# Kernel optimization log

Measured on AMD Instinct MI355X. Metric: run time of the kernel, lower is better.

## Reference

```python
import jax, jax.numpy as jnp
import numpy as np

EPS_IN = 1e-5   # torch InstanceNorm2d default eps
EPS_VAR = 1e-6  # clamp floor on attention-weighted variance


def _inorm(x):
    # x: (b, c, t); InstanceNorm2d with affine=False normalizes over spatial dims
    m = x.mean(axis=-1, keepdims=True)
    v = x.var(axis=-1, keepdims=True)  # biased variance, matches torch eval-mode IN
    return (x - m) / jnp.sqrt(v + EPS_IN)


def setup_inputs() -> dict:
    key = jax.random.key(0)
    ks = jax.random.split(key, 9)
    b, t, d = 4, 4096, 256
    sc = 1.0 / np.sqrt(d).astype(np.float32)
    return {
        "fc": jax.random.normal(ks[0], (b, t, d), jnp.float32),
        "fs": jax.random.normal(ks[1], (b, t, d), jnp.float32),
        "fcs": jax.random.normal(ks[2], (b, t, d), jnp.float32),
        "Wf": jax.random.normal(ks[3], (d, d), jnp.float32) * sc,
        "bf": jax.random.normal(ks[4], (d,), jnp.float32) * 0.01,
        "Wg": jax.random.normal(ks[5], (d, d), jnp.float32) * sc,
        "bg": jax.random.normal(ks[6], (d,), jnp.float32) * 0.01,
        "Wh": jax.random.normal(ks[7], (d, d), jnp.float32) * sc,
        "bh": jax.random.normal(ks[8], (d,), jnp.float32) * 0.01,
    }


def reference(fc, fs, fcs, Wf, bf, Wg, bg, Wh, bh):
    # (b, t, d) -> channel-first flat (b, d, t); 1x1 conv == per-token linear
    fc_t = jnp.swapaxes(fc, 1, 2)
    fs_t = jnp.swapaxes(fs, 1, 2)
    fcs_t = jnp.swapaxes(fcs, 1, 2)

    Q = jnp.einsum('oc,bct->bto', Wf, _inorm(fc_t)) + bf                 # (b,t,d)
    K = jnp.einsum('oc,bct->bot', Wg, _inorm(fs_t)) + bg[None, :, None]  # (b,d,t)
    V = jnp.einsum('oc,bct->bto', Wh, fs_t) + bh                         # (b,t,d)

    A = jax.nn.softmax(jnp.einsum('btd,bdu->btu', Q, K), axis=-1)        # (b,t,t)
    M = jnp.einsum('btu,bud->btd', A, V)                                 # mean
    Var = jnp.einsum('btu,bud->btd', A, V * V) - M * M                   # E[v^2]-E[v]^2
    S = jnp.sqrt(jnp.maximum(Var, EPS_VAR))

    out_t = jnp.swapaxes(S, 1, 2) * _inorm(fcs_t) + jnp.swapaxes(M, 1, 2)  # (b,d,t)
    return jnp.swapaxes(out_t, 1, 2)  # (b, t, d)
```

## Files before the change

kernel.cpp:

```cpp
#include <hip/hip_runtime.h>
#include <math.h>

#define B 4
#define T 4096
#define D 256
#define NCH 16
#define CHT (T / NCH)
#define KC 32
#define NCHUNK (T / KC)

typedef __attribute__((ext_vector_type(8))) _Float16 half8;
typedef __attribute__((ext_vector_type(4))) _Float16 half4;
typedef __attribute__((ext_vector_type(4))) float f32x4;

__global__ __launch_bounds__(256) void k_stats_part(
    const float* __restrict__ fc, const float* __restrict__ fs,
    const float* __restrict__ fcs, float* __restrict__ part)
{
    int blk = blockIdx.x;
    int tensor = blk / (B * NCH);
    int rem = blk % (B * NCH);
    int b = rem / NCH, ch = rem % NCH;
    const float* x = (tensor == 0) ? fc : ((tensor == 1) ? fs : fcs);
    int c = threadIdx.x;
    const float* p = x + ((size_t)b * T + (size_t)ch * CHT) * D + c;
    float s = 0.f, ss = 0.f;
    for (int t = 0; t < CHT; ++t) {
        float v = p[(size_t)t * D];
        s += v; ss += v * v;
    }
    float* o = part + (((size_t)tensor * B + b) * NCH + ch) * 2 * D;
    o[c] = s;
    o[D + c] = ss;
}

__global__ __launch_bounds__(256) void k_stats_final(
    const float* __restrict__ part, float* __restrict__ stats)
{
    int blk = blockIdx.x;
    int tensor = blk / B, b = blk % B;
    int c = threadIdx.x;
    const float* pp = part + (((size_t)tensor * B + b) * NCH) * 2 * D;
    float s = 0.f, ss = 0.f;
    for (int ch = 0; ch < NCH; ++ch) {
        s  += pp[(size_t)ch * 2 * D + c];
        ss += pp[(size_t)ch * 2 * D + D + c];
    }
    float mean = s / (float)T;
    float var  = ss / (float)T - mean * mean;
    float rstd = rsqrtf(var + 1e-5f);
    float* st = stats + (size_t)tensor * 2 * B * D;
    st[(size_t)b * D + c]          = mean;
    st[(size_t)B * D + b * D + c]  = rstd;
}

__global__ __launch_bounds__(256) void k_wprep(
    const float* __restrict__ Wf, const float* __restrict__ Wg,
    const float* __restrict__ Wh, _Float16* __restrict__ Whi,
    _Float16* __restrict__ Wlo)
{
    int blk = blockIdx.x;
    int which = blk >> 8, row = blk & 255;
    const float* Wsrc = (which == 0) ? Wf : ((which == 1) ? Wg : Wh);
    int c = threadIdx.x;
    float v = Wsrc[row * 256 + c];
    _Float16 h = (_Float16)v;
    float l = v - (float)h;
    size_t off = ((size_t)which << 16) + (row << 8) + c;
    Whi[off] = h;
    Wlo[off] = (_Float16)l;
}

__global__ __launch_bounds__(256) void k_gemm_mfma(
    const float* __restrict__ x, const _Float16* __restrict__ Whi,
    const _Float16* __restrict__ Wlo, const float* __restrict__ bias,
    const float* __restrict__ stats, int use_norm, int mode,
    _Float16* __restrict__ out1,
    _Float16* __restrict__ oV, _Float16* __restrict__ oV2h,
    _Float16* __restrict__ oV2l)
{
    __shared__ _Float16 Xl[64 * 256];
    int m0 = blockIdx.x * 64;
    int b = m0 / T;
    int tid = threadIdx.x;
    const float* mean = stats;
    const float* rstd = stats + B * D;

    #pragma unroll
    for (int j = 0; j < 16; ++j) {
        int idx = tid + j * 256;
        int m = idx >> 6, c4 = idx & 63;
        float4 v = *(const float4*)(x + ((size_t)(m0 + m)) * D + c4 * 4);
        if (use_norm) {
            int c = c4 * 4;
            v.x = (v.x - mean[b * D + c + 0]) * rstd[b * D + c + 0];
            v.y = (v.y - mean[b * D + c + 1]) * rstd[b * D + c + 1];
            v.z = (v.z - mean[b * D + c + 2]) * rstd[b * D + c + 2];
            v.w = (v.w - mean[b * D + c + 3]) * rstd[b * D + c + 3];
        }
        half4 h;
        h[0] = (_Float16)v.x; h[1] = (_Float16)v.y;
        h[2] = (_Float16)v.z; h[3] = (_Float16)v.w;
        *(half4*)&Xl[m * 256 + ((c4 * 4) ^ ((m & 7) << 3))] = h;
    }
    __syncthreads();

    const int l = tid & 63, w = tid >> 6;
    const int lo16 = l & 15, hi4 = l >> 4;
    const int row = w * 16 + lo16;

    float bias_v[16];
    #pragma unroll
    for (int nt = 0; nt < 16; ++nt) bias_v[nt] = bias[nt * 16 + lo16];

    f32x4 acc[16];
    #pragma unroll
    for (int nt = 0; nt < 16; ++nt) acc[nt] = (f32x4){0.f, 0.f, 0.f, 0.f};

    #pragma unroll
    for (int kk = 0; kk < 8; ++kk) {
        half8 a = *(const half8*)&Xl[row * 256 + ((kk * 32 + hi4 * 8) ^ ((row & 7) << 3))];
        #pragma unroll
        for (int nt = 0; nt < 16; ++nt) {
            size_t wo = (size_t)(nt * 16 + lo16) * 256 + kk * 32 + hi4 * 8;
            half8 bh = *(const half8*)(Whi + wo);
            acc[nt] = __builtin_amdgcn_mfma_f32_16x16x32_f16(a, bh, acc[nt], 0, 0, 0);
            half8 bl = *(const half8*)(Wlo + wo);
            acc[nt] = __builtin_amdgcn_mfma_f32_16x16x32_f16(a, bl, acc[nt], 0, 0, 0);
        }
    }

    if (mode == 1) {
        #pragma unroll
        for (int nt = 0; nt < 16; ++nt)
            #pragma unroll
            for (int r = 0; r < 4; ++r) {
                int t = m0 + w * 16 + hi4 * 4 + r;
                out1[(size_t)t * D + nt * 16 + lo16] = (_Float16)(acc[nt][r] + bias_v[nt]);
            }
    } else {
        int t0 = (m0 % T) + w * 16 + hi4 * 4;
        #pragma unroll
        for (int nt = 0; nt < 16; ++nt) {
            int o = nt * 16 + lo16;
            half4 vh, h4, l4;
            #pragma unroll
            for (int r = 0; r < 4; ++r) {
                float v = acc[nt][r] + bias_v[nt];
                _Float16 vhh = (_Float16)v;
                float f2 = (float)vhh * (float)vhh;
                _Float16 hh = (_Float16)f2;
                float fl = f2 - (float)hh;
                vh[r] = vhh; h4[r] = hh; l4[r] = (_Float16)fl;
            }
            size_t base = ((size_t)b * D + o) * T + t0;
            *(half4*)(oV   + base) = vh;
            *(half4*)(oV2h + base) = h4;
            *(half4*)(oV2l + base) = l4;
        }
    }
}

__global__ __launch_bounds__(512, 2) void k_attn(
    const _Float16* __restrict__ Qg, const _Float16* __restrict__ Kg,
    const _Float16* __restrict__ Vtg, const _Float16* __restrict__ V2hg,
    const _Float16* __restrict__ V2lg, const float* __restrict__ fcs,
    const float* __restrict__ stats_fcs, float* __restrict__ out)
{
    __shared__ __align__(16) _Float16 Kl [2][32 * 256];
    __shared__ __align__(16) _Float16 Vl [2][256 * 32];
    __shared__ __align__(16) _Float16 V2h[2][256 * 32];
    __shared__ __align__(16) _Float16 V2l[2][256 * 32];
    __shared__ __align__(16) _Float16 Pl[64 * 32];
    __shared__ float corr_lds[64];
    __shared__ float l_lds[64];
    __shared__ int   flags[4];

    const int tid = threadIdx.x;
    const int l = tid & 63;
    const int w = tid >> 6;
    const int b  = blockIdx.x >> 6;
    const int q0 = (blockIdx.x & 63) << 6;
    const int lo16 = l & 15, hi4 = l >> 4;

    const _Float16* KgB  = Kg   + (size_t)b * T * D;
    const _Float16* VtB  = Vtg  + (size_t)b * D * T;
    const _Float16* V2hB = V2hg + (size_t)b * D * T;
    const _Float16* V2lB = V2lg + (size_t)b * D * T;

    half8 qf[8];
    if (w < 4) {
        const _Float16* qp = Qg + ((size_t)(b * T + q0 + 16 * w + lo16)) * D + hi4 * 8;
        #pragma unroll
        for (int kk = 0; kk < 8; ++kk) qf[kk] = *(const half8*)(qp + kk * 32);
    }

    f32x4 accM[4][2], accE[4][2];
    #pragma unroll
    for (int qs = 0; qs < 4; ++qs)
        #pragma unroll
        for (int jj = 0; jj < 2; ++jj) {
            accM[qs][jj] = (f32x4){0.f, 0.f, 0.f, 0.f};
            accE[qs][jj] = (f32x4){0.f, 0.f, 0.f, 0.f};
        }
    float m_run[4] = {-1e9f, -1e9f, -1e9f, -1e9f};
    float lv[4] = {0.f, 0.f, 0.f, 0.f};

    auto stage = [&](int kcs, int cb) {
        int k0 = kcs * KC;
        int t2 = tid & 255;
        half8 kr[4], vr[4], vhr[4], vlr[4];
        #pragma unroll
        for (int i = 0; i < 4; ++i) {
            int g = t2 + i * 256;
            kr[i] = *(const half8*)(KgB + (size_t)(k0 + (g >> 5)) * D + (g & 31) * 8);
        }
        #pragma unroll
        for (int i = 0; i < 4; ++i) {
            int g = t2 + i * 256; int d = g >> 2, kg = g & 3;
            size_t off = (size_t)d * T + k0 + kg * 8;
            vr[i]  = *(const half8*)(VtB  + off);
            vhr[i] = *(const half8*)(V2hB + off);
            vlr[i] = *(const half8*)(V2lB + off);
        }
        #pragma unroll
        for (int i = 0; i < 4; ++i) {
            int g = t2 + i * 256; int rr = g >> 5, cg = g & 31;
            *(half8*)&Kl[cb][rr * 256 + ((cg ^ (rr & 7)) << 3)] = kr[i];
        }
        #pragma unroll
        for (int i = 0; i < 4; ++i) {
            int g = t2 + i * 256; int d = g >> 2, kg = g & 3;
            int p = d * 32 + ((kg ^ ((d >> 1) & 3)) << 3);
            *(half8*)&Vl[cb][p]  = vr[i];
            *(half8*)&V2h[cb][p] = vhr[i];
            *(half8*)&V2l[cb][p] = vlr[i];
        }
    };

    if (w >= 4) stage(0, 0);
    __syncthreads();
    int cur = 0;

    for (int kc = 0; kc < NCHUNK; ++kc) {
        if (w < 4) {
            f32x4 c0 = (f32x4){0.f, 0.f, 0.f, 0.f}, c1 = (f32x4){0.f, 0.f, 0.f, 0.f};
            #pragma unroll
            for (int kk = 0; kk < 8; ++kk) {
                int cg = kk * 4 + hi4;
                half8 b0 = *(const half8*)&Kl[cur][lo16 * 256 + ((cg ^ (lo16 & 7)) << 3)];
                half8 b1 = *(const half8*)&Kl[cur][(16 + lo16) * 256 + ((cg ^ ((16 + lo16) & 7)) << 3)];
                c0 = __builtin_amdgcn_mfma_f32_16x16x32_f16(qf[kk], b0, c0, 0, 0, 0);
                c1 = __builtin_amdgcn_mfma_f32_16x16x32_f16(qf[kk], b1, c1, 0, 0, 0);
            }

            float cm[4];
            #pragma unroll
            for (int r = 0; r < 4; ++r) cm[r] = fmaxf(c0[r], c1[r]);
            float tmax = fmaxf(fmaxf(cm[0] - m_run[0], cm[1] - m_run[1]),
                               fmaxf(cm[2] - m_run[2], cm[3] - m_run[3]));
            int flagv = 0;
            if (__any(tmax > 10.f)) {
                flagv = 1;
                float corr[4];
                #pragma unroll
                for (int r = 0; r < 4; ++r) {
                    float rm = cm[r];
                    rm = fmaxf(rm, __shfl_xor(rm, 1));
                    rm = fmaxf(rm, __shfl_xor(rm, 2));
                    rm = fmaxf(rm, __shfl_xor(rm, 4));
                    rm = fmaxf(rm, __shfl_xor(rm, 8));
                    float mn = fmaxf(m_run[r], rm);
                    corr[r] = __expf(m_run[r] - mn);
                    m_run[r] = mn;
                    lv[r] *= corr[r];
                }
                if (lo16 == 0) {
                    #pragma unroll
                    for (int r = 0; r < 4; ++r)
                        corr_lds[w * 16 + hi4 * 4 + r] = corr[r];
                }
            }
            if (l == 0) flags[w] = flagv;

            float p0[4], p1[4];
            #pragma unroll
            for (int r = 0; r < 4; ++r) {
                p0[r] = __expf(c0[r] - m_run[r]);
                p1[r] = __expf(c1[r] - m_run[r]);
                lv[r] += p0[r] + p1[r];
            }
            #pragma unroll
            for (int r = 0; r < 4; ++r) {
                int q = 16 * w + hi4 * 4 + r;
                int ka = lo16, kb = 16 + lo16;
                Pl[q * 32 + (((ka >> 3) ^ (q & 3)) << 3) + (ka & 7)] = (_Float16)p0[r];
                Pl[q * 32 + (((kb >> 3) ^ (q & 3)) << 3) + (kb & 7)] = (_Float16)p1[r];
            }
        } else {
            if (kc + 1 < NCHUNK) stage(kc + 1, cur ^ 1);
        }
        __syncthreads();

        #pragma unroll
        for (int qs = 0; qs < 4; ++qs) {
            if (flags[qs]) {
                #pragma unroll
                for (int r = 0; r < 4; ++r) {
                    float c = corr_lds[qs * 16 + hi4 * 4 + r];
                    accM[qs][0][r] *= c; accM[qs][1][r] *= c;
                    accE[qs][0][r] *= c; accE[qs][1][r] *= c;
                }
            }
        }

        half8 pa[4];
        #pragma unroll
        for (int qs = 0; qs < 4; ++qs) {
            int q = qs * 16 + lo16;
            pa[qs] = *(const half8*)&Pl[q * 32 + ((hi4 ^ (q & 3)) << 3)];
        }

        #pragma unroll
        for (int jj = 0; jj < 2; ++jj) {
            int d = (2 * w + jj) * 16 + lo16;
            int p = d * 32 + ((hi4 ^ ((d >> 1) & 3)) << 3);
            half8 bh  = *(const half8*)&Vl[cur][p];
            half8 b2h = *(const half8*)&V2h[cur][p];
            half8 b2l = *(const half8*)&V2l[cur][p];
            #pragma unroll
            for (int qs = 0; qs < 4; ++qs) {
                accM[qs][jj] = __builtin_amdgcn_mfma_f32_16x16x32_f16(pa[qs], bh,  accM[qs][jj], 0, 0, 0);
                accE[qs][jj] = __builtin_amdgcn_mfma_f32_16x16x32_f16(pa[qs], b2h, accE[qs][jj], 0, 0, 0);
                accE[qs][jj] = __builtin_amdgcn_mfma_f32_16x16x32_f16(pa[qs], b2l, accE[qs][jj], 0, 0, 0);
            }
        }

        __syncthreads();
        cur ^= 1;
    }

    if (w < 4) {
        #pragma unroll
        for (int r = 0; r < 4; ++r) {
            float lr = lv[r];
            lr += __shfl_xor(lr, 1);
            lr += __shfl_xor(lr, 2);
            lr += __shfl_xor(lr, 4);
            lr += __shfl_xor(lr, 8);
            if (lo16 == 0) l_lds[w * 16 + hi4 * 4 + r] = lr;
        }
    }
    __syncthreads();

    const float* mfc = stats_fcs;
    const float* rfc = stats_fcs + B * D;
    #pragma unroll
    for (int qs = 0; qs < 4; ++qs) {
        #pragma unroll
        for (int r = 0; r < 4; ++r) {
            float linv = 1.f / l_lds[qs * 16 + hi4 * 4 + r];
            int q = q0 + qs * 16 + hi4 * 4 + r;
            size_t rowb = ((size_t)(b * T + q)) * D;
            #pragma unroll
            for (int jj = 0; jj < 2; ++jj) {
                int d = (2 * w + jj) * 16 + lo16;
                float M  = accM[qs][jj][r] * linv;
                float E2 = accE[qs][jj][r] * linv;
                float S  = sqrtf(fmaxf(E2 - M * M, 1e-6f));
                float f  = fcs[rowb + d];
                out[rowb + d] = S * ((f - mfc[b * D + d]) * rfc[b * D + d]) + M;
            }
        }
    }
}

extern "C" void kernel_launch(void* const* d_in, const int* in_sizes, int n_in,
                              void* d_out, int out_size, void* d_ws, size_t ws_size,
                              hipStream_t stream)
{
    const float* fc  = (const float*)d_in[0];
    const float* fs  = (const float*)d_in[1];
    const float* fcs = (const float*)d_in[2];
    const float* Wf  = (const float*)d_in[3];
    const float* bf  = (const float*)d_in[4];
    const float* Wg  = (const float*)d_in[5];
    const float* bg  = (const float*)d_in[6];
    const float* Wh  = (const float*)d_in[7];
    const float* bh  = (const float*)d_in[8];
    float* out = (float*)d_out;

    char* ws = (char*)d_ws;
    float* stats = (float*)ws;
    float* part  = (float*)(ws + (64 << 10));
    _Float16* Whi = (_Float16*)(ws + (512 << 10));
    _Float16* Wlo = Whi + 3 * 65536;
    _Float16* Qg   = (_Float16*)(ws + (2 << 20));
    _Float16* Kg   = Qg  + (size_t)B * T * D;
    _Float16* Vtg  = Kg  + (size_t)B * T * D;
    _Float16* V2hg = Vtg + (size_t)B * T * D;
    _Float16* V2lg = V2hg + (size_t)B * T * D;

    k_stats_part<<<3 * B * NCH, 256, 0, stream>>>(fc, fs, fcs, part);
    k_stats_final<<<3 * B, 256, 0, stream>>>(part, stats);
    k_wprep<<<3 * 256, 256, 0, stream>>>(Wf, Wg, Wh, Whi, Wlo);

    float* st_fc  = stats + 0 * 2 * B * D;
    float* st_fs  = stats + 1 * 2 * B * D;
    float* st_fcs = stats + 2 * 2 * B * D;

    k_gemm_mfma<<<(B * T) / 64, 256, 0, stream>>>(fc, Whi,             Wlo,             bf, st_fc, 1, 1, Qg, nullptr, nullptr, nullptr);
    k_gemm_mfma<<<(B * T) / 64, 256, 0, stream>>>(fs, Whi + 65536,     Wlo + 65536,     bg, st_fs, 1, 1, Kg, nullptr, nullptr, nullptr);
    k_gemm_mfma<<<(B * T) / 64, 256, 0, stream>>>(fs, Whi + 2 * 65536, Wlo + 2 * 65536, bh, st_fs, 0, 2, nullptr, Vtg, V2hg, V2lg);

    k_attn<<<B * (T / 64), 512, 0, stream>>>(Qg, Kg, Vtg, V2hg, V2lg, fcs, st_fcs, out);
}
```

Measured before the change: 366.2 us.

## Stream K/V tiles straight into LDS with global_load_lds and single buffering

Drops the register-staged, producer-warp double buffer for K, V, V2h and V2l. All warps now issue direct global-to-LDS 16-byte loads into single-buffered tiles. K for the next chunk is issued after the first barrier, and V for the current chunk at the start of the iteration. Halving the LDS footprint lets launch bounds rise to four blocks per CU, so other blocks' occupancy can hide latency. In exchange, a block no longer overlaps its own loads with compute, and correctness relies on the loads completing before each barrier.

```diff
diff --git a/kernel.cpp b/kernel.cpp
--- a/kernel.cpp
+++ b/kernel.cpp
@@ -12,6 +12,12 @@
 typedef __attribute__((ext_vector_type(8))) _Float16 half8;
 typedef __attribute__((ext_vector_type(4))) _Float16 half4;
 typedef __attribute__((ext_vector_type(4))) float f32x4;
+
+__device__ inline void gload16(const void* g, void* l) {
+    __builtin_amdgcn_global_load_lds(
+        (const __attribute__((address_space(1))) void*)g,
+        (__attribute__((address_space(3))) void*)l, 16, 0, 0);
+}
 
 __global__ __launch_bounds__(256) void k_stats_part(
     const float* __restrict__ fc, const float* __restrict__ fs,
@@ -161,16 +167,16 @@
     }
 }
 
-__global__ __launch_bounds__(512, 2) void k_attn(
+__global__ __launch_bounds__(512, 4) void k_attn(
     const _Float16* __restrict__ Qg, const _Float16* __restrict__ Kg,
     const _Float16* __restrict__ Vtg, const _Float16* __restrict__ V2hg,
     const _Float16* __restrict__ V2lg, const float* __restrict__ fcs,
     const float* __restrict__ stats_fcs, float* __restrict__ out)
 {
-    __shared__ __align__(16) _Float16 Kl [2][32 * 256];
-    __shared__ __align__(16) _Float16 Vl [2][256 * 32];
-    __shared__ __align__(16) _Float16 V2h[2][256 * 32];
-    __shared__ __align__(16) _Float16 V2l[2][256 * 32];
+    __shared__ __align__(16) _Float16 Kl [32 * 256];
+    __shared__ __align__(16) _Float16 Vl [256 * 32];
+    __shared__ __align__(16) _Float16 V2h[256 * 32];
+    __shared__ __align__(16) _Float16 V2l[256 * 32];
     __shared__ __align__(16) _Float16 Pl[64 * 32];
     __shared__ float corr_lds[64];
     __shared__ float l_lds[64];
@@ -206,50 +212,46 @@
     float m_run[4] = {-1e9f, -1e9f, -1e9f, -1e9f};
     float lv[4] = {0.f, 0.f, 0.f, 0.f};
 
-    auto stage = [&](int kcs, int cb) {
-        int k0 = kcs * KC;
-        int t2 = tid & 255;
-        half8 kr[4], vr[4], vhr[4], vlr[4];
-        #pragma unroll
-        for (int i = 0; i < 4; ++i) {
-            int g = t2 + i * 256;
-            kr[i] = *(const half8*)(KgB + (size_t)(k0 + (g >> 5)) * D + (g & 31) * 8);
-        }
-        #pragma unroll
-        for (int i = 0; i < 4; ++i) {
-            int g = t2 + i * 256; int d = g >> 2, kg = g & 3;
-            size_t off = (size_t)d * T + k0 + kg * 8;
-            vr[i]  = *(const half8*)(VtB  + off);
-            vhr[i] = *(const half8*)(V2hB + off);
-            vlr[i] = *(const half8*)(V2lB + off);
-        }
-        #pragma unroll
-        for (int i = 0; i < 4; ++i) {
-            int g = t2 + i * 256; int rr = g >> 5, cg = g & 31;
-            *(half8*)&Kl[cb][rr * 256 + ((cg ^ (rr & 7)) << 3)] = kr[i];
-        }
-        #pragma unroll
-        for (int i = 0; i < 4; ++i) {
-            int g = t2 + i * 256; int d = g >> 2, kg = g & 3;
-            int p = d * 32 + ((kg ^ ((d >> 1) & 3)) << 3);
-            *(half8*)&Vl[cb][p]  = vr[i];
-            *(half8*)&V2h[cb][p] = vhr[i];
-            *(half8*)&V2l[cb][p] = vlr[i];
+    auto issueK = [&](int kc) {
+        int k0 = kc * KC;
+        #pragma unroll
+        for (int i = 0; i < 2; ++i) {
+            int u = (w * 2 + i) * 64 + l;
+            int row = u >> 5;
+            int pg = u & 31;
+            int cg = pg ^ (row & 7);
+            gload16(KgB + (size_t)(k0 + row) * D + cg * 8,
+                    Kl + (size_t)((w * 2 + i) * 512));
         }
     };
-
-    if (w >= 4) stage(0, 0);
+    auto issueV = [&](int kc) {
+        int k0 = kc * KC;
+        #pragma unroll
+        for (int i = 0; i < 2; ++i) {
+            int u = (w * 2 + i) * 64 + l;
+            int d = u >> 2;
+            int pg = u & 3;
+            int kg = pg ^ ((d >> 1) & 3);
+            size_t soff = (size_t)d * T + k0 + kg * 8;
+            size_t dbase = (size_t)((w * 2 + i) * 512);
+            gload16(VtB  + soff, Vl  + dbase);
+            gload16(V2hB + soff, V2h + dbase);
+            gload16(V2lB + soff, V2l + dbase);
+        }
+    };
+
+    issueK(0);
     __syncthreads();
-    int cur = 0;
 
     for (int kc = 0; kc < NCHUNK; ++kc) {
+        issueV(kc);
         if (w < 4) {
             f32x4 c0 = (f32x4){0.f, 0.f, 0.f, 0.f}, c1 = (f32x4){0.f, 0.f, 0.f, 0.f};
             #pragma unroll
             for (int kk = 0; kk < 8; ++kk) {
                 int cg = kk * 4 + hi4;
-                half8 b0 = *(const half8*)&Kl[cur][lo16 * 256 + ((cg ^ (lo16 & 7)) << 3)];
-                half8 b1 = *(const half8*)&Kl[cur][(16 + lo16) * 256 + ((cg ^ ((16 + lo16) & 7)) << 3)];
+                half8 b0 = *(const half8*)&Kl[lo16 * 256 + ((cg ^ (lo16 & 7)) << 3)];
+                half8 b1 = *(const half8*)&Kl[(16 + lo16) * 256 + ((cg ^ ((16 + lo16) & 7)) << 3)];
                 c0 = __builtin_amdgcn_mfma_f32_16x16x32_f16(qf[kk], b0, c0, 0, 0, 0);
                 c1 = __builtin_amdgcn_mfma_f32_16x16x32_f16(qf[kk], b1, c1, 0, 0, 0);
             }
@@ -297,10 +299,10 @@
                 Pl[q * 32 + (((ka >> 3) ^ (q & 3)) << 3) + (ka & 7)] = (_Float16)p0[r];
                 Pl[q * 32 + (((kb >> 3) ^ (q & 3)) << 3) + (kb & 7)] = (_Float16)p1[r];
             }
-        } else {
-            if (kc + 1 < NCHUNK) stage(kc + 1, cur ^ 1);
         }
         __syncthreads();
+
+        if (kc + 1 < NCHUNK) issueK(kc + 1);
 
         #pragma unroll
         for (int qs = 0; qs < 4; ++qs) {
@@ -325,9 +327,9 @@
         for (int jj = 0; jj < 2; ++jj) {
             int d = (2 * w + jj) * 16 + lo16;
             int p = d * 32 + ((hi4 ^ ((d >> 1) & 3)) << 3);
-            half8 bh  = *(const half8*)&Vl[cur][p];
-            half8 b2h = *(const half8*)&V2h[cur][p];
-            half8 b2l = *(const half8*)&V2l[cur][p];
+            half8 bh  = *(const half8*)&Vl[p];
+            half8 b2h = *(const half8*)&V2h[p];
+            half8 b2l = *(const half8*)&V2l[p];
             #pragma unroll
             for (int qs = 0; qs < 4; ++qs) {
                 accM[qs][jj] = __builtin_amdgcn_mfma_f32_16x16x32_f16(pa[qs], bh,  accM[qs][jj], 0, 0, 0);
@@ -337,7 +339,6 @@
         }
 
         __syncthreads();
-        cur ^= 1;
     }
 
     if (w < 4) {
```

After: 702.4 us. 1.92x slower.

## Shrink attention blocks to 32 queries and single-buffer LDS with overlapped staging

Applied to the files above, without the earlier changes.

Each attention block now handles 32 queries with 256 threads instead of 64 queries with 512, which doubles the grid to 512 blocks. Block indices are swizzled across batches. The double-buffered LDS is replaced by single buffers: V for the current chunk is staged by the loader waves while the compute waves do QK^T, and K for the next chunk is prefetched into registers during the PV MFMAs and written after them. The aim is to cut the LDS footprint and raise occupancy and parallelism. In exchange, each block rereads the full K/V stream for fewer queries, doubling global and L2 traffic, and V staging now sits on the critical path.

```diff
diff --git a/kernel.cpp b/kernel.cpp
--- a/kernel.cpp
+++ b/kernel.cpp
@@ -161,26 +161,29 @@
     }
 }
 
-__global__ __launch_bounds__(512, 2) void k_attn(
+__global__ __launch_bounds__(256, 2) void k_attn(
     const _Float16* __restrict__ Qg, const _Float16* __restrict__ Kg,
     const _Float16* __restrict__ Vtg, const _Float16* __restrict__ V2hg,
     const _Float16* __restrict__ V2lg, const float* __restrict__ fcs,
     const float* __restrict__ stats_fcs, float* __restrict__ out)
 {
-    __shared__ __align__(16) _Float16 Kl [2][32 * 256];
-    __shared__ __align__(16) _Float16 Vl [2][256 * 32];
-    __shared__ __align__(16) _Float16 V2h[2][256 * 32];
-    __shared__ __align__(16) _Float16 V2l[2][256 * 32];
-    __shared__ __align__(16) _Float16 Pl[64 * 32];
-    __shared__ float corr_lds[64];
-    __shared__ float l_lds[64];
-    __shared__ int   flags[4];
+    __shared__ __align__(16) _Float16 Kl [32 * 256];
+    __shared__ __align__(16) _Float16 Vl [256 * 32];
+    __shared__ __align__(16) _Float16 V2h[256 * 32];
+    __shared__ __align__(16) _Float16 V2l[256 * 32];
+    __shared__ __align__(16) _Float16 Pl[32 * 32];
+    __shared__ float corr_lds[32];
+    __shared__ float l_lds[32];
+    __shared__ int   flags[2];
 
     const int tid = threadIdx.x;
     const int l = tid & 63;
     const int w = tid >> 6;
-    const int b  = blockIdx.x >> 6;
-    const int q0 = (blockIdx.x & 63) << 6;
+    const int t2 = tid & 127;
+
+    int swz = (blockIdx.x & 7) * 64 + (blockIdx.x >> 3);
+    const int b  = swz >> 7;
+    const int q0 = (swz & 127) << 5;
     const int lo16 = l & 15, hi4 = l >> 4;
 
     const _Float16* KgB  = Kg   + (size_t)b * T * D;
@@ -189,67 +192,71 @@
     const _Float16* V2lB = V2lg + (size_t)b * D * T;
 
     half8 qf[8];
-    if (w < 4) {
+    if (w < 2) {
         const _Float16* qp = Qg + ((size_t)(b * T + q0 + 16 * w + lo16)) * D + hi4 * 8;
         #pragma unroll
         for (int kk = 0; kk < 8; ++kk) qf[kk] = *(const half8*)(qp + kk * 32);
     }
 
-    f32x4 accM[4][2], accE[4][2];
-    #pragma unroll
-    for (int qs = 0; qs < 4; ++qs)
-        #pragma unroll
-        for (int jj = 0; jj < 2; ++jj) {
+    f32x4 accM[2][4], accE[2][4];
+    #pragma unroll
+    for (int qs = 0; qs < 2; ++qs)
+        #pragma unroll
+        for (int jj = 0; jj < 4; ++jj) {
             accM[qs][jj] = (f32x4){0.f, 0.f, 0.f, 0.f};
             accE[qs][jj] = (f32x4){0.f, 0.f, 0.f, 0.f};
         }
     float m_run[4] = {-1e9f, -1e9f, -1e9f, -1e9f};
     float lv[4] = {0.f, 0.f, 0.f, 0.f};
 
-    auto stage = [&](int kcs, int cb) {
-        int k0 = kcs * KC;
-        int t2 = tid & 255;
-        half8 kr[4], vr[4], vhr[4], vlr[4];
-        #pragma unroll
-        for (int i = 0; i < 4; ++i) {
-            int g = t2 + i * 256;
-            kr[i] = *(const half8*)(KgB + (size_t)(k0 + (g >> 5)) * D + (g & 31) * 8);
-        }
-        #pragma unroll
-        for (int i = 0; i < 4; ++i) {
-            int g = t2 + i * 256; int d = g >> 2, kg = g & 3;
-            size_t off = (size_t)d * T + k0 + kg * 8;
-            vr[i]  = *(const half8*)(VtB  + off);
-            vhr[i] = *(const half8*)(V2hB + off);
-            vlr[i] = *(const half8*)(V2lB + off);
-        }
-        #pragma unroll
-        for (int i = 0; i < 4; ++i) {
-            int g = t2 + i * 256; int rr = g >> 5, cg = g & 31;
-            *(half8*)&Kl[cb][rr * 256 + ((cg ^ (rr & 7)) << 3)] = kr[i];
-        }
-        #pragma unroll
-        for (int i = 0; i < 4; ++i) {
-            int g = t2 + i * 256; int d = g >> 2, kg = g & 3;
-            int p = d * 32 + ((kg ^ ((d >> 1) & 3)) << 3);
-            *(half8*)&Vl[cb][p]  = vr[i];
-            *(half8*)&V2h[cb][p] = vhr[i];
-            *(half8*)&V2l[cb][p] = vlr[i];
+    auto stageV = [&](int kc) {
+        int k0 = kc * KC;
+        #pragma unroll
+        for (int rnd = 0; rnd < 2; ++rnd) {
+            half8 vr[4], vhr[4], vlr[4];
+            #pragma unroll
+            for (int i = 0; i < 4; ++i) {
+                int g = t2 + (rnd * 4 + i) * 128;
+                size_t off = (size_t)(g >> 2) * T + k0 + (g & 3) * 8;
+                vr[i]  = *(const half8*)(VtB  + off);
+                vhr[i] = *(const half8*)(V2hB + off);
+                vlr[i] = *(const half8*)(V2lB + off);
+            }
+            #pragma unroll
+            for (int i = 0; i < 4; ++i) {
+                int g = t2 + (rnd * 4 + i) * 128;
+                int d = g >> 2, kg = g & 3;
+                int p = d * 32 + ((kg ^ ((d >> 1) & 3)) << 3);
+                *(half8*)&Vl[p]  = vr[i];
+                *(half8*)&V2h[p] = vhr[i];
+                *(half8*)&V2l[p] = vlr[i];
+            }
         }
     };
 
-    if (w >= 4) stage(0, 0);
+    if (w >= 2) {
+        half8 kr[8];
+        #pragma unroll
+        for (int i = 0; i < 8; ++i) {
+            int g = t2 + i * 128;
+            kr[i] = *(const half8*)(KgB + (size_t)(g >> 5) * D + (g & 31) * 8);
+        }
+        #pragma unroll
+        for (int i = 0; i < 8; ++i) {
+            int g = t2 + i * 128; int rr = g >> 5, cg = g & 31;
+            *(half8*)&Kl[rr * 256 + ((cg ^ (rr & 7)) << 3)] = kr[i];
+        }
+    }
     __syncthreads();
-    int cur = 0;
 
     for (int kc = 0; kc < NCHUNK; ++kc) {
-        if (w < 4) {
+        if (w < 2) {
             f32x4 c0 = (f32x4){0.f, 0.f, 0.f, 0.f}, c1 = (f32x4){0.f, 0.f, 0.f, 0.f};
             #pragma unroll
             for (int kk = 0; kk < 8; ++kk) {
                 int cg = kk * 4 + hi4;
-                half8 b0 = *(const half8*)&Kl[cur][lo16 * 256 + ((cg ^ (lo16 & 7)) << 3)];
-                half8 b1 = *(const half8*)&Kl[cur][(16 + lo16) * 256 + ((cg ^ ((16 + lo16) & 7)) << 3)];
+                half8 b0 = *(const half8*)&Kl[lo16 * 256 + ((cg ^ (lo16 & 7)) << 3)];
+                half8 b1 = *(const half8*)&Kl[(16 + lo16) * 256 + ((cg ^ ((16 + lo16) & 7)) << 3)];
                 c0 = __builtin_amdgcn_mfma_f32_16x16x32_f16(qf[kk], b0, c0, 0, 0, 0);
                 c1 = __builtin_amdgcn_mfma_f32_16x16x32_f16(qf[kk], b1, c1, 0, 0, 0);
             }
@@ -298,49 +305,66 @@
                 Pl[q * 32 + (((kb >> 3) ^ (q & 3)) << 3) + (kb & 7)] = (_Float16)p1[r];
             }
         } else {
-            if (kc + 1 < NCHUNK) stage(kc + 1, cur ^ 1);
+            stageV(kc);
         }
         __syncthreads();
 
-        #pragma unroll
-        for (int qs = 0; qs < 4; ++qs) {
+        half8 kr[8];
+        const bool doK = (w >= 2) && (kc + 1 < NCHUNK);
+        if (doK) {
+            int k0 = (kc + 1) * KC;
+            #pragma unroll
+            for (int i = 0; i < 8; ++i) {
+                int g = t2 + i * 128;
+                kr[i] = *(const half8*)(KgB + (size_t)(k0 + (g >> 5)) * D + (g & 31) * 8);
+            }
+        }
+
+        #pragma unroll
+        for (int qs = 0; qs < 2; ++qs) {
             if (flags[qs]) {
                 #pragma unroll
                 for (int r = 0; r < 4; ++r) {
                     float c = corr_lds[qs * 16 + hi4 * 4 + r];
-                    accM[qs][0][r] *= c; accM[qs][1][r] *= c;
-                    accE[qs][0][r] *= c; accE[qs][1][r] *= c;
+                    #pragma unroll
+                    for (int jj = 0; jj < 4; ++jj) { accM[qs][jj][r] *= c; accE[qs][jj][r] *= c; }
                 }
             }
         }
 
-        half8 pa[4];
-        #pragma unroll
-        for (int qs = 0; qs < 4; ++qs) {
+        half8 pa[2];
+        #pragma unroll
+        for (int qs = 0; qs < 2; ++qs) {
             int q = qs * 16 + lo16;
             pa[qs] = *(const half8*)&Pl[q * 32 + ((hi4 ^ (q & 3)) << 3)];
         }
 
         #pragma unroll
-        for (int jj = 0; jj < 2; ++jj) {
-            int d = (2 * w + jj) * 16 + lo16;
+        for (int jj = 0; jj < 4; ++jj) {
+            int d = (4 * w + jj) * 16 + lo16;
             int p = d * 32 + ((hi4 ^ ((d >> 1) & 3)) << 3);
-            half8 bh  = *(const half8*)&Vl[cur][p];
-            half8 b2h = *(const half8*)&V2h[cur][p];
-            half8 b2l = *(const half8*)&V2l[cur][p];
-            #pragma unroll
-            for (int qs = 0; qs < 4; ++qs) {
+            half8 bh  = *(const half8*)&Vl[p];
+            half8 b2h = *(const half8*)&V2h[p];
+            half8 b2l = *(const half8*)&V2l[p];
+            #pragma unroll
+            for (int qs = 0; qs < 2; ++qs) {
                 accM[qs][jj] = __builtin_amdgcn_mfma_f32_16x16x32_f16(pa[qs], bh,  accM[qs][jj], 0, 0, 0);
                 accE[qs][jj] = __builtin_amdgcn_mfma_f32_16x16x32_f16(pa[qs], b2h, accE[qs][jj], 0, 0, 0);
                 accE[qs][jj] = __builtin_amdgcn_mfma_f32_16x16x32_f16(pa[qs], b2l, accE[qs][jj], 0, 0, 0);
             }
         }
 
+        if (doK) {
+            #pragma unroll
+            for (int i = 0; i < 8; ++i) {
+                int g = t2 + i * 128; int rr = g >> 5, cg = g & 31;
+                *(half8*)&Kl[rr * 256 + ((cg ^ (rr & 7)) << 3)] = kr[i];
+            }
+        }
         __syncthreads();
-        cur ^= 1;
-    }
-
-    if (w < 4) {
+    }
+
+    if (w < 2) {
         #pragma unroll
         for (int r = 0; r < 4; ++r) {
             float lr = lv[r];
@@ -356,15 +380,15 @@
     const float* mfc = stats_fcs;
     const float* rfc = stats_fcs + B * D;
     #pragma unroll
-    for (int qs = 0; qs < 4; ++qs) {
+    for (int qs = 0; qs < 2; ++qs) {
         #pragma unroll
         for (int r = 0; r < 4; ++r) {
             float linv = 1.f / l_lds[qs * 16 + hi4 * 4 + r];
             int q = q0 + qs * 16 + hi4 * 4 + r;
             size_t rowb = ((size_t)(b * T + q)) * D;
             #pragma unroll
-            for (int jj = 0; jj < 2; ++jj) {
-                int d = (2 * w + jj) * 16 + lo16;
+            for (int jj = 0; jj < 4; ++jj) {
+                int d = (4 * w + jj) * 16 + lo16;
                 float M  = accM[qs][jj][r] * linv;
                 float E2 = accE[qs][jj][r] * linv;
                 float S  = sqrtf(fmaxf(E2 - M * M, 1e-6f));
@@ -413,5 +437,5 @@
     k_gemm_mfma<<<(B * T) / 64, 256, 0, stream>>>(fs, Whi + 65536,     Wlo + 65536,     bg, st_fs, 1, 1, Kg, nullptr, nullptr, nullptr);
     k_gemm_mfma<<<(B * T) / 64, 256, 0, stream>>>(fs, Whi + 2 * 65536, Wlo + 2 * 65536, bh, st_fs, 0, 2, nullptr, Vtg, V2hg, V2lg);
 
-    k_attn<<<B * (T / 64), 512, 0, stream>>>(Qg, Kg, Vtg, V2hg, V2lg, fcs, st_fcs, out);
-}
+    k_attn<<<B * (T / 32), 256, 0, stream>>>(Qg, Kg, Vtg, V2hg, V2lg, fcs, st_fcs, out);
+}
```

Result: slower. 381.1 us (+4.1%).
